# Kernel tuning notes

Measured on AMD Instinct MI355X. Metric: run time of the kernel, lower is better.

## Reference

```python
import jax, jax.numpy as jnp
import numpy as np

B, H, W, C = 32, 56, 56, 128
K_WINNERS = 40141  # round(0.1 * 56*56*128)


def setup_inputs() -> dict:
    key = jax.random.key(0)
    k1, k2 = jax.random.split(key)
    x = jax.random.normal(k1, (B, H, W, C), dtype=jnp.float32)
    duty_cycles = jax.random.uniform(k2, (1, 1, 1, C), dtype=jnp.float32)
    boost_strength = jnp.ones((), dtype=jnp.float32)
    return {
        "x": x,
        "duty_cycles": duty_cycles,
        "boost_strength": boost_strength,
        "k": K_WINNERS,
    }


def reference(x, duty_cycles, boost_strength, k):
    # Faithful to compute_kwinners: boost -> top-k over flattened units ->
    # binary mask (scatter == one_hot+reduce_sum since top-k indices are
    # unique) -> apply mask to UNboosted activations.
    batch = x.shape[0]
    n = int(np.prod(x.shape[1:]))
    bs = jnp.maximum(boost_strength, 0.0)
    target_density = jnp.float32(k) / jnp.float32(n)
    boost_factors = jnp.exp((target_density - duty_cycles) * bs)  # [1,1,1,C]
    boosted = (x * boost_factors).reshape(batch, n)  # [B, n]
    flat_x = x.reshape(batch, n)
    _, idx = jax.lax.top_k(boosted, k)  # idx: [B, k], unique per row
    rows = jnp.arange(batch)[:, None]
    mask = jnp.zeros_like(flat_x).at[rows, idx].set(1.0)
    return (mask * flat_x).reshape(x.shape)
```

## Files before the change

### kernel.cpp

```cpp
#include <hip/hip_runtime.h>
#include <math.h>

#define NROW 32
#define NPR  401408
#define N4   100352
#define NCH  128
#define NBIN 4096
#define NBLK 64
#define GRID (NROW*NBLK)
#define CHUNK (N4/NBLK)
#define SCAP 1024
#define LCAP 1024
#define TCAP 1024

#define OFF_BF    0
#define OFF_ST    512
#define OFF_TCNT  1024
#define OFF_BCNT  2048
#define OFF_H1    16384
#define OFF_H2    (OFF_H1 + 4*NBIN*NROW)
#define OFF_TIE   (OFF_H2 + 4*NBIN*NROW)
#define OFF_EQ    (OFF_TIE + 8*TCAP*NROW)
#define ZSTART    OFF_TCNT
#define ZWORDS    ((OFF_TIE - OFF_TCNT)/4)

__device__ __forceinline__ unsigned sortkey(float f) {
    unsigned u = __float_as_uint(f);
    return (u & 0x80000000u) ? ~u : (u | 0x80000000u);
}

__device__ __forceinline__ void rscan(const unsigned* __restrict__ gh, unsigned target,
                                      volatile unsigned* warr, volatile unsigned* outv) {
    int tid = threadIdx.x, lane = tid & 63, w = tid >> 6;
    unsigned hv[16], s = 0;
    int p0 = tid * 16;
#pragma unroll
    for (int q = 0; q < 16; ++q) { unsigned c = gh[4095 - (p0 + q)]; hv[q] = c; s += c; }
    unsigned inc = s;
#pragma unroll
    for (int d = 1; d < 64; d <<= 1) { unsigned o = __shfl_up(inc, d, 64); if (lane >= d) inc += o; }
    if (lane == 63) warr[w] = inc;
    __syncthreads();
    unsigned cum = inc - s;
    for (int ww = 0; ww < w; ++ww) cum += warr[ww];
#pragma unroll
    for (int q = 0; q < 16; ++q) {
        unsigned c = hv[q];
        if (cum < target && cum + c >= target) { outv[0] = (unsigned)(4095 - (p0 + q)); outv[1] = target - cum; }
        cum += c;
    }
    __syncthreads();
}

__global__ void k_prep(unsigned* z, int nwords, const float* duty, const float* bsp,
                       const int* kp, float* bf) {
    int i = blockIdx.x * 256 + threadIdx.x;
    if (i < nwords) z[i] = 0;
    if (blockIdx.x == 0 && threadIdx.x < NCH) {
        float bs = fmaxf(bsp[0], 0.0f);
        float td = (float)kp[0] / (float)NPR;
        bf[threadIdx.x] = (float)exp((double)((td - duty[threadIdx.x]) * bs));
    }
}

__global__ __launch_bounds__(256, 8) void k_hist(const float* __restrict__ x,
                                                 const float* __restrict__ bf,
                                                 unsigned* __restrict__ h1) {
    __shared__ unsigned h[NBIN];
    __shared__ float bfs[NCH];
    int tid = threadIdx.x;
    for (int i = tid; i < NBIN; i += 256) h[i] = 0;
    if (tid < NCH) bfs[tid] = bf[tid];
    __syncthreads();
    int row = blockIdx.x >> 6, bx = blockIdx.x & 63;
    const float4* xr = (const float4*)(x + (size_t)row * NPR) + (size_t)bx * CHUNK;
    int base = bx * CHUNK * 4;
    for (int i = tid; i < CHUNK; i += 256) {
        float4 v = xr[i];
        int c = (base + i * 4) & (NCH - 1);
        atomicAdd(&h[sortkey(v.x * bfs[c])     >> 20], 1u);
        atomicAdd(&h[sortkey(v.y * bfs[c + 1]) >> 20], 1u);
        atomicAdd(&h[sortkey(v.z * bfs[c + 2]) >> 20], 1u);
        atomicAdd(&h[sortkey(v.w * bfs[c + 3]) >> 20], 1u);
    }
    __syncthreads();
    unsigned* gh = h1 + (size_t)row * NBIN;
    for (int i = tid; i < NBIN; i += 256) {
        unsigned s = h[i];
        if (s) atomicAdd(&gh[i], s);
    }
}

__global__ __launch_bounds__(256, 4) void k_collect(const float* __restrict__ x,
                                                    const float* __restrict__ bf,
                                                    const int* __restrict__ kp,
                                                    const unsigned* __restrict__ h1,
                                                    unsigned* __restrict__ h2,
                                                    unsigned* __restrict__ bcnt,
                                                    uint2* __restrict__ eq) {
    __shared__ float bfs[NCH];
    __shared__ unsigned h[NBIN];
    __shared__ uint2 stage[LCAP];
    __shared__ unsigned warr[4];
    __shared__ unsigned outv[2];
    __shared__ unsigned scnt;
    int tid = threadIdx.x;
    if (tid < NCH) bfs[tid] = bf[tid];
    for (int i = tid; i < NBIN; i += 256) h[i] = 0;
    if (tid == 0) scnt = 0;
    int row = blockIdx.x >> 6, bx = blockIdx.x & 63;
    __syncthreads();
    rscan(h1 + (size_t)row * NBIN, (unsigned)kp[0], warr, outv);
    unsigned p1 = outv[0];

    const float4* xr = (const float4*)(x + (size_t)row * NPR) + (size_t)bx * CHUNK;
    int base = bx * CHUNK * 4;
    uint2* slice = eq + (size_t)blockIdx.x * SCAP;
    for (int i = tid; i < CHUNK; i += 256) {
        float4 v = xr[i];
        int j = base + i * 4;
        int c = j & (NCH - 1);
        unsigned kk[4] = { sortkey(v.x * bfs[c]),     sortkey(v.y * bfs[c + 1]),
                           sortkey(v.z * bfs[c + 2]), sortkey(v.w * bfs[c + 3]) };
#pragma unroll
        for (int t = 0; t < 4; ++t) {
            if ((kk[t] >> 20) == p1) {
                atomicAdd(&h[(kk[t] >> 8) & 0xFFFu], 1u);
                unsigned pos = atomicAdd(&scnt, 1u);
                uint2 e = make_uint2((unsigned)(j + t), kk[t]);
                if (pos < LCAP) stage[pos] = e;
                else if (pos < SCAP) slice[pos] = e;
            }
        }
    }
    __syncthreads();
    unsigned m = min(scnt, (unsigned)LCAP);
    for (unsigned i = tid; i < m; i += 256) slice[i] = stage[i];
    if (tid == 0) bcnt[blockIdx.x] = min(scnt, (unsigned)SCAP);
    unsigned* gh = h2 + (size_t)row * NBIN;
    for (int i = tid; i < NBIN; i += 256)
        if (h[i]) atomicAdd(&gh[i], h[i]);
}

__global__ __launch_bounds__(256, 4) void k_selectA(const unsigned* __restrict__ h1,
                                                    const unsigned* __restrict__ h2,
                                                    const int* __restrict__ kp,
                                                    const unsigned* __restrict__ bcnt,
                                                    const uint2* __restrict__ eq,
                                                    unsigned* __restrict__ stout,
                                                    unsigned* __restrict__ tcnt,
                                                    uint2* __restrict__ tie) {
    __shared__ unsigned warr[4];
    __shared__ unsigned outv[2];
    int tid = threadIdx.x;
    int row = blockIdx.x >> 6;
    rscan(h1 + (size_t)row * NBIN, (unsigned)kp[0], warr, outv);
    unsigned p1 = outv[0], krem1 = outv[1];
    __syncthreads();
    rscan(h2 + (size_t)row * NBIN, krem1, warr, outv);
    unsigned p2 = outv[0], krem2 = outv[1];
    unsigned pref = (p1 << 12) | p2;
    if (tid == 0) { stout[row * 2] = krem2; stout[row * 2 + 1] = pref; }
    unsigned m = bcnt[blockIdx.x];
    const uint2* sl = eq + (size_t)blockIdx.x * SCAP;
    for (unsigned i = tid; i < m; i += 256) {
        uint2 e = sl[i];
        if ((e.y >> 8) == pref) {
            unsigned pos = atomicAdd(&tcnt[row], 1u);
            if (pos < TCAP) tie[(size_t)row * TCAP + pos] = e;
        }
    }
}

__global__ __launch_bounds__(256, 8) void k_mask(const float* __restrict__ x,
                                                 const float* __restrict__ bf,
                                                 const unsigned* __restrict__ stout,
                                                 const unsigned* __restrict__ tcnt,
                                                 const uint2* __restrict__ tie,
                                                 float* __restrict__ out) {
    __shared__ float bfs[NCH];
    __shared__ uint2 stie[TCAP];
    __shared__ unsigned res[2];
    int tid = threadIdx.x;
    int row = blockIdx.x >> 6, bx = blockIdx.x & 63;
    if (tid < NCH) bfs[tid] = bf[tid];
    unsigned krem2 = stout[row * 2];
    unsigned tm = min(tcnt[row], (unsigned)TCAP);
    for (unsigned i = tid; i < tm; i += 256) stie[i] = tie[(size_t)row * TCAP + i];
    __syncthreads();
    for (unsigned i = tid; i < tm; i += 256) {
        uint2 e = stie[i];
        unsigned r = 0;
        for (unsigned j = 0; j < tm; ++j) {
            uint2 f = stie[j];
            r += (f.y > e.y) || (f.y == e.y && f.x < e.x);
        }
        if (r == krem2 - 1) { res[0] = e.y; res[1] = e.x; }
    }
    __syncthreads();
    unsigned tkey = res[0], cutoff = res[1];

    const float4* xr = (const float4*)(x + (size_t)row * NPR) + (size_t)bx * CHUNK;
    float4* outr = (float4*)(out + (size_t)row * NPR) + (size_t)bx * CHUNK;
    int base = bx * CHUNK * 4;
    for (int i = tid; i < CHUNK; i += 256) {
        float4 v = xr[i];
        int j = base + i * 4;
        int c = j & (NCH - 1);
        unsigned k0 = sortkey(v.x * bfs[c]);
        unsigned k1 = sortkey(v.y * bfs[c + 1]);
        unsigned k2 = sortkey(v.z * bfs[c + 2]);
        unsigned k3 = sortkey(v.w * bfs[c + 3]);
        float4 o;
        o.x = (k0 > tkey || (k0 == tkey && (unsigned)(j + 0) <= cutoff)) ? v.x : 0.0f;
        o.y = (k1 > tkey || (k1 == tkey && (unsigned)(j + 1) <= cutoff)) ? v.y : 0.0f;
        o.z = (k2 > tkey || (k2 == tkey && (unsigned)(j + 2) <= cutoff)) ? v.z : 0.0f;
        o.w = (k3 > tkey || (k3 == tkey && (unsigned)(j + 3) <= cutoff)) ? v.w : 0.0f;
        outr[i] = o;
    }
}

extern "C" void kernel_launch(void* const* d_in, const int* in_sizes, int n_in,
                              void* d_out, int out_size, void* d_ws, size_t ws_size,
                              hipStream_t stream) {
    const float* x    = (const float*)d_in[0];
    const float* duty = (const float*)d_in[1];
    const float* bsp  = (const float*)d_in[2];
    const int*   kp   = (const int*)d_in[3];
    float* out = (float*)d_out;

    char* ws = (char*)d_ws;
    float*    bf   = (float*)(ws + OFF_BF);
    unsigned* st   = (unsigned*)(ws + OFF_ST);
    unsigned* tcnt = (unsigned*)(ws + OFF_TCNT);
    unsigned* bcnt = (unsigned*)(ws + OFF_BCNT);
    unsigned* h1   = (unsigned*)(ws + OFF_H1);
    unsigned* h2   = (unsigned*)(ws + OFF_H2);
    uint2*    tie  = (uint2*)(ws + OFF_TIE);
    uint2*    eq   = (uint2*)(ws + OFF_EQ);

    k_prep<<<(ZWORDS + 255) / 256, 256, 0, stream>>>((unsigned*)(ws + ZSTART), ZWORDS,
                                                     duty, bsp, kp, bf);
    k_hist<<<GRID, 256, 0, stream>>>(x, bf, h1);
    k_collect<<<GRID, 256, 0, stream>>>(x, bf, kp, h1, h2, bcnt, eq);
    k_selectA<<<GRID, 256, 0, stream>>>(h1, h2, kp, bcnt, eq, st, tcnt, tie);
    k_mask<<<GRID, 256, 0, stream>>>(x, bf, st, tcnt, tie, out);
}
```

Before: 145.9 us.

## Use 56 blocks per row with fixed unrolled loops and packed 16-bit LDS histograms

```diff
diff --git a/kernel.cpp b/kernel.cpp
--- a/kernel.cpp
+++ b/kernel.cpp
@@ -6,7 +6,7 @@
 #define N4   100352
 #define NCH  128
 #define NBIN 4096
-#define NBLK 64
+#define NBLK 56
 #define GRID (NROW*NBLK)
 #define CHUNK (N4/NBLK)
 #define SCAP 1024
@@ -66,32 +66,39 @@
 __global__ __launch_bounds__(256, 8) void k_hist(const float* __restrict__ x,
                                                  const float* __restrict__ bf,
                                                  unsigned* __restrict__ h1) {
-    __shared__ unsigned h[NBIN];
+    __shared__ unsigned hp[NBIN / 2];
     __shared__ float bfs[NCH];
     int tid = threadIdx.x;
-    for (int i = tid; i < NBIN; i += 256) h[i] = 0;
+    for (int i = tid; i < NBIN / 2; i += 256) hp[i] = 0;
     if (tid < NCH) bfs[tid] = bf[tid];
     __syncthreads();
-    int row = blockIdx.x >> 6, bx = blockIdx.x & 63;
+    int row = blockIdx.x / NBLK, bx = blockIdx.x % NBLK;
     const float4* xr = (const float4*)(x + (size_t)row * NPR) + (size_t)bx * CHUNK;
     int base = bx * CHUNK * 4;
-    for (int i = tid; i < CHUNK; i += 256) {
-        float4 v = xr[i];
-        int c = (base + i * 4) & (NCH - 1);
-        atomicAdd(&h[sortkey(v.x * bfs[c])     >> 20], 1u);
-        atomicAdd(&h[sortkey(v.y * bfs[c + 1]) >> 20], 1u);
-        atomicAdd(&h[sortkey(v.z * bfs[c + 2]) >> 20], 1u);
-        atomicAdd(&h[sortkey(v.w * bfs[c + 3]) >> 20], 1u);
+    int c = (base + tid * 4) & (NCH - 1);
+    float b0 = bfs[c], b1 = bfs[c + 1], b2 = bfs[c + 2], b3 = bfs[c + 3];
+#pragma unroll
+    for (int m = 0; m < CHUNK / 256; ++m) {
+        float4 v = xr[tid + m * 256];
+        unsigned k0 = sortkey(v.x * b0) >> 20;
+        unsigned k1 = sortkey(v.y * b1) >> 20;
+        unsigned k2 = sortkey(v.z * b2) >> 20;
+        unsigned k3 = sortkey(v.w * b3) >> 20;
+        atomicAdd(&hp[k0 >> 1], 1u << ((k0 & 1) << 4));
+        atomicAdd(&hp[k1 >> 1], 1u << ((k1 & 1) << 4));
+        atomicAdd(&hp[k2 >> 1], 1u << ((k2 & 1) << 4));
+        atomicAdd(&hp[k3 >> 1], 1u << ((k3 & 1) << 4));
     }
     __syncthreads();
     unsigned* gh = h1 + (size_t)row * NBIN;
-    for (int i = tid; i < NBIN; i += 256) {
-        unsigned s = h[i];
-        if (s) atomicAdd(&gh[i], s);
-    }
-}
-
-__global__ __launch_bounds__(256, 4) void k_collect(const float* __restrict__ x,
+    for (int i = tid; i < NBIN / 2; i += 256) {
+        unsigned p = hp[i];
+        if (p & 0xFFFFu) atomicAdd(&gh[2 * i], p & 0xFFFFu);
+        if (p >> 16)     atomicAdd(&gh[2 * i + 1], p >> 16);
+    }
+}
+
+__global__ __launch_bounds__(256, 6) void k_collect(const float* __restrict__ x,
                                                     const float* __restrict__ bf,
                                                     const int* __restrict__ kp,
                                                     const unsigned* __restrict__ h1,
@@ -99,16 +106,16 @@
                                                     unsigned* __restrict__ bcnt,
                                                     uint2* __restrict__ eq) {
     __shared__ float bfs[NCH];
-    __shared__ unsigned h[NBIN];
+    __shared__ unsigned hp[NBIN / 2];
     __shared__ uint2 stage[LCAP];
     __shared__ unsigned warr[4];
     __shared__ unsigned outv[2];
     __shared__ unsigned scnt;
     int tid = threadIdx.x;
     if (tid < NCH) bfs[tid] = bf[tid];
-    for (int i = tid; i < NBIN; i += 256) h[i] = 0;
+    for (int i = tid; i < NBIN / 2; i += 256) hp[i] = 0;
     if (tid == 0) scnt = 0;
-    int row = blockIdx.x >> 6, bx = blockIdx.x & 63;
+    int row = blockIdx.x / NBLK, bx = blockIdx.x % NBLK;
     __syncthreads();
     rscan(h1 + (size_t)row * NBIN, (unsigned)kp[0], warr, outv);
     unsigned p1 = outv[0];
@@ -116,16 +123,19 @@
     const float4* xr = (const float4*)(x + (size_t)row * NPR) + (size_t)bx * CHUNK;
     int base = bx * CHUNK * 4;
     uint2* slice = eq + (size_t)blockIdx.x * SCAP;
-    for (int i = tid; i < CHUNK; i += 256) {
-        float4 v = xr[i];
-        int j = base + i * 4;
-        int c = j & (NCH - 1);
-        unsigned kk[4] = { sortkey(v.x * bfs[c]),     sortkey(v.y * bfs[c + 1]),
-                           sortkey(v.z * bfs[c + 2]), sortkey(v.w * bfs[c + 3]) };
+    int cch = (base + tid * 4) & (NCH - 1);
+    float b0 = bfs[cch], b1 = bfs[cch + 1], b2 = bfs[cch + 2], b3 = bfs[cch + 3];
+#pragma unroll
+    for (int m = 0; m < CHUNK / 256; ++m) {
+        float4 v = xr[tid + m * 256];
+        int j = base + (tid + m * 256) * 4;
+        unsigned kk[4] = { sortkey(v.x * b0), sortkey(v.y * b1),
+                           sortkey(v.z * b2), sortkey(v.w * b3) };
 #pragma unroll
         for (int t = 0; t < 4; ++t) {
             if ((kk[t] >> 20) == p1) {
-                atomicAdd(&h[(kk[t] >> 8) & 0xFFFu], 1u);
+                unsigned b2i = (kk[t] >> 8) & 0xFFFu;
+                atomicAdd(&hp[b2i >> 1], 1u << ((b2i & 1) << 4));
                 unsigned pos = atomicAdd(&scnt, 1u);
                 uint2 e = make_uint2((unsigned)(j + t), kk[t]);
                 if (pos < LCAP) stage[pos] = e;
@@ -134,12 +144,15 @@
         }
     }
     __syncthreads();
-    unsigned m = min(scnt, (unsigned)LCAP);
-    for (unsigned i = tid; i < m; i += 256) slice[i] = stage[i];
+    unsigned m2 = min(scnt, (unsigned)LCAP);
+    for (unsigned i = tid; i < m2; i += 256) slice[i] = stage[i];
     if (tid == 0) bcnt[blockIdx.x] = min(scnt, (unsigned)SCAP);
     unsigned* gh = h2 + (size_t)row * NBIN;
-    for (int i = tid; i < NBIN; i += 256)
-        if (h[i]) atomicAdd(&gh[i], h[i]);
+    for (int i = tid; i < NBIN / 2; i += 256) {
+        unsigned p = hp[i];
+        if (p & 0xFFFFu) atomicAdd(&gh[2 * i], p & 0xFFFFu);
+        if (p >> 16)     atomicAdd(&gh[2 * i + 1], p >> 16);
+    }
 }
 
 __global__ __launch_bounds__(256, 4) void k_selectA(const unsigned* __restrict__ h1,
@@ -147,20 +160,18 @@
                                                     const int* __restrict__ kp,
                                                     const unsigned* __restrict__ bcnt,
                                                     const uint2* __restrict__ eq,
-                                                    unsigned* __restrict__ stout,
                                                     unsigned* __restrict__ tcnt,
                                                     uint2* __restrict__ tie) {
     __shared__ unsigned warr[4];
     __shared__ unsigned outv[2];
     int tid = threadIdx.x;
-    int row = blockIdx.x >> 6;
+    int row = blockIdx.x / NBLK;
     rscan(h1 + (size_t)row * NBIN, (unsigned)kp[0], warr, outv);
     unsigned p1 = outv[0], krem1 = outv[1];
     __syncthreads();
     rscan(h2 + (size_t)row * NBIN, krem1, warr, outv);
-    unsigned p2 = outv[0], krem2 = outv[1];
+    unsigned p2 = outv[0];
     unsigned pref = (p1 << 12) | p2;
-    if (tid == 0) { stout[row * 2] = krem2; stout[row * 2 + 1] = pref; }
     unsigned m = bcnt[blockIdx.x];
     const uint2* sl = eq + (size_t)blockIdx.x * SCAP;
     for (unsigned i = tid; i < m; i += 256) {
@@ -174,17 +185,27 @@
 
 __global__ __launch_bounds__(256, 8) void k_mask(const float* __restrict__ x,
                                                  const float* __restrict__ bf,
-                                                 const unsigned* __restrict__ stout,
+                                                 const int* __restrict__ kp,
+                                                 const unsigned* __restrict__ h1,
+                                                 const unsigned* __restrict__ h2,
                                                  const unsigned* __restrict__ tcnt,
                                                  const uint2* __restrict__ tie,
                                                  float* __restrict__ out) {
     __shared__ float bfs[NCH];
     __shared__ uint2 stie[TCAP];
+    __shared__ unsigned warr[4];
+    __shared__ unsigned outv[2];
     __shared__ unsigned res[2];
     int tid = threadIdx.x;
-    int row = blockIdx.x >> 6, bx = blockIdx.x & 63;
+    int row = blockIdx.x / NBLK, bx = blockIdx.x % NBLK;
     if (tid < NCH) bfs[tid] = bf[tid];
-    unsigned krem2 = stout[row * 2];
+    __syncthreads();
+    rscan(h1 + (size_t)row * NBIN, (unsigned)kp[0], warr, outv);
+    unsigned p1 = outv[0], krem1 = outv[1];
+    __syncthreads();
+    rscan(h2 + (size_t)row * NBIN, krem1, warr, outv);
+    unsigned p2 = outv[0], krem2 = outv[1];
+    unsigned pref = (p1 << 12) | p2;
     unsigned tm = min(tcnt[row], (unsigned)TCAP);
     for (unsigned i = tid; i < tm; i += 256) stie[i] = tie[(size_t)row * TCAP + i];
     __syncthreads();
@@ -199,24 +220,27 @@
     }
     __syncthreads();
     unsigned tkey = res[0], cutoff = res[1];
+    (void)pref;
 
     const float4* xr = (const float4*)(x + (size_t)row * NPR) + (size_t)bx * CHUNK;
     float4* outr = (float4*)(out + (size_t)row * NPR) + (size_t)bx * CHUNK;
     int base = bx * CHUNK * 4;
-    for (int i = tid; i < CHUNK; i += 256) {
-        float4 v = xr[i];
-        int j = base + i * 4;
-        int c = j & (NCH - 1);
-        unsigned k0 = sortkey(v.x * bfs[c]);
-        unsigned k1 = sortkey(v.y * bfs[c + 1]);
-        unsigned k2 = sortkey(v.z * bfs[c + 2]);
-        unsigned k3 = sortkey(v.w * bfs[c + 3]);
+    int cch = (base + tid * 4) & (NCH - 1);
+    float b0 = bfs[cch], b1 = bfs[cch + 1], b2 = bfs[cch + 2], b3 = bfs[cch + 3];
+#pragma unroll
+    for (int m = 0; m < CHUNK / 256; ++m) {
+        float4 v = xr[tid + m * 256];
+        int j = base + (tid + m * 256) * 4;
+        unsigned k0 = sortkey(v.x * b0);
+        unsigned k1 = sortkey(v.y * b1);
+        unsigned k2 = sortkey(v.z * b2);
+        unsigned k3 = sortkey(v.w * b3);
         float4 o;
         o.x = (k0 > tkey || (k0 == tkey && (unsigned)(j + 0) <= cutoff)) ? v.x : 0.0f;
         o.y = (k1 > tkey || (k1 == tkey && (unsigned)(j + 1) <= cutoff)) ? v.y : 0.0f;
         o.z = (k2 > tkey || (k2 == tkey && (unsigned)(j + 2) <= cutoff)) ? v.z : 0.0f;
         o.w = (k3 > tkey || (k3 == tkey && (unsigned)(j + 3) <= cutoff)) ? v.w : 0.0f;
-        outr[i] = o;
+        outr[tid + m * 256] = o;
     }
 }
 
@@ -231,7 +255,6 @@
 
     char* ws = (char*)d_ws;
     float*    bf   = (float*)(ws + OFF_BF);
-    unsigned* st   = (unsigned*)(ws + OFF_ST);
     unsigned* tcnt = (unsigned*)(ws + OFF_TCNT);
     unsigned* bcnt = (unsigned*)(ws + OFF_BCNT);
     unsigned* h1   = (unsigned*)(ws + OFF_H1);
@@ -243,6 +266,6 @@
                                                      duty, bsp, kp, bf);
     k_hist<<<GRID, 256, 0, stream>>>(x, bf, h1);
     k_collect<<<GRID, 256, 0, stream>>>(x, bf, kp, h1, h2, bcnt, eq);
-    k_selectA<<<GRID, 256, 0, stream>>>(h1, h2, kp, bcnt, eq, st, tcnt, tie);
-    k_mask<<<GRID, 256, 0, stream>>>(x, bf, st, tcnt, tie, out);
-}
+    k_selectA<<<GRID, 256, 0, stream>>>(h1, h2, kp, bcnt, eq, tcnt, tie);
+    k_mask<<<GRID, 256, 0, stream>>>(x, bf, kp, h1, h2, tcnt, tie, out);
+}
```

Result: no change. 144.8 us (-0.7%).
